# Performance work log

Hardware: AMD Instinct MI355X
Metric: run time of the kernel (lower is better)

## Reference

```python
import jax, jax.numpy as jnp
import numpy as np

N_NODES = 10000
N_EDGES = 160000
MUL = 128          # channel multiplicity
N_SPECIES = 10
SH_OFF = [0, 1, 4, 9, 16]   # spherical-harmonic offsets for l=0..3 (2l+1 each)
RADIAL_IN = 8
SIN_DIM = 32
MAX_DENSITY = 100.0


def setup_inputs() -> dict:
    key = jax.random.key(0)
    ks = jax.random.split(key, 16)
    inp = {
        'node_attrs': jax.random.normal(ks[0], (N_NODES, N_SPECIES), jnp.float32),
        'node_feats': jax.random.normal(ks[1], (N_NODES, MUL), jnp.float32),
        'edge_attrs': jax.random.normal(ks[2], (N_EDGES, 16), jnp.float32),
        'edge_feats': jax.random.normal(ks[3], (N_EDGES, RADIAL_IN), jnp.float32),
        'edge_index': jax.random.randint(ks[4], (2, N_EDGES), 0, N_NODES, jnp.int64),
        'W_up': jax.random.normal(ks[5], (MUL, MUL), jnp.float32),
        'Wr1': jax.random.normal(ks[6], (RADIAL_IN, 64), jnp.float32),
        'Wr2': jax.random.normal(ks[7], (64, 64), jnp.float32),
        'Wr3': jax.random.normal(ks[8], (64, 64), jnp.float32),
        'Wr4': jax.random.normal(ks[9], (64, 4 * MUL), jnp.float32),
        'Wd': jax.random.normal(ks[10], (RADIAL_IN, 1), jnp.float32),
        'Wsin': jax.random.normal(ks[11], (SIN_DIM, MUL), jnp.float32),
        'Wlin': jax.random.normal(ks[12], (4, MUL, MUL), jnp.float32),
        'Wskip': jax.random.normal(ks[13], (4, MUL, N_SPECIES, MUL), jnp.float32),
    }
    return inp


def _sinusoidal_embedding(x):
    # continuous sinusoidal embedding: dim=32, max_density=100
    half = SIN_DIM // 2
    freqs = jnp.exp(-jnp.log(MAX_DENSITY) * jnp.arange(half, dtype=x.dtype) / half)
    ang = x[:, None] * freqs[None, :]          # [N, 16]
    return jnp.concatenate([jnp.sin(ang), jnp.cos(ang)], axis=-1)  # [N, 32]


def reference(node_attrs, node_feats, edge_attrs, edge_feats, edge_index,
              W_up, Wr1, Wr2, Wr3, Wr4, Wd, Wsin, Wlin, Wskip):
    N = node_feats.shape[0]
    sender, receiver = edge_index[0], edge_index[1]

    # linear_up (e3nn o3.Linear on 128x0e, fan-in normalized)
    x = node_feats @ (W_up / np.float32(np.sqrt(MUL)))          # [N, 128]

    # radial MLP: FullyConnectedNet([8,64,64,64,512], silu), fan-in normalized
    h = edge_feats
    for W in (Wr1, Wr2, Wr3):
        h = jax.nn.silu(h @ (W / np.float32(np.sqrt(W.shape[0]))))
    tp_w = (h @ (Wr4 / np.float32(np.sqrt(64)))).reshape(-1, 4, MUL)  # [E, 4, 128]

    # equivariant TP: scalar node feats (x) gathered by sender, uvu path per SH l
    xs = x[sender]                                              # [E, 128]
    weighted = xs[:, None, :] * tp_w                            # [E, 4, 128]
    blocks = []
    for l in range(4):
        sh_l = edge_attrs[:, SH_OFF[l]:SH_OFF[l + 1]]           # [E, 2l+1]
        blk = weighted[:, l, :, None] * sh_l[:, None, :]        # [E, 128, 2l+1]
        blocks.append(blk.reshape(blk.shape[0], -1))
    mji = jnp.concatenate(blocks, axis=-1)                      # [E, 2048]

    # per-edge density gate
    density = jnp.tanh((edge_feats @ Wd) ** 2)                  # [E, 1]

    # scatter-sum messages and density to receivers
    message = jax.ops.segment_sum(mji, receiver, num_segments=N)        # [N, 2048]
    rho = jax.ops.segment_sum(density, receiver, num_segments=N)       # [N, 1]
    message = message / (rho + 1.0)

    # density embedding injected into the l=0 block
    demb = _sinusoidal_embedding(rho[:, 0]) @ Wsin              # [N, 128]
    message = message.at[:, :MUL].add(demb)

    # per-l linear (irreps_mid -> irreps_out), skip_tp with node_attrs, reshape
    out_blocks = []
    for l in range(4):
        d = 2 * l + 1
        blk = message[:, MUL * SH_OFF[l]:MUL * SH_OFF[l + 1]].reshape(N, MUL, d)
        blk = jnp.einsum('nuk,uv->nvk', blk, Wlin[l]) / np.float32(np.sqrt(MUL))
        blk = jnp.einsum('nvk,na,vaw->nwk', blk, node_attrs, Wskip[l]) \
              / np.float32(np.sqrt(MUL * N_SPECIES))
        out_blocks.append(blk)
    return jnp.concatenate(out_blocks, axis=-1)                 # [N, 128, 16]
```

## Files before the change

### kernel.cpp

```cpp
#include <hip/hip_runtime.h>
#include <hip/hip_bf16.h>

#define N_NODES 10000
#define N_EDGES 160000

typedef _Float16 h8 __attribute__((ext_vector_type(8)));
typedef _Float16 h4 __attribute__((ext_vector_type(4)));
typedef _Float16 h2 __attribute__((ext_vector_type(2)));
typedef float f32x4 __attribute__((ext_vector_type(4)));

__device__ __forceinline__ float silu_f(float v){ return v / (1.f + expf(-v)); }

__global__ __launch_bounds__(256) void k_node_up(const float* __restrict__ nf,
                                                 const _Float16* __restrict__ WupT,
                                                 float* __restrict__ x){
  const int n0 = blockIdx.x * 64;
  const int tid = threadIdx.x;
  alignas(16) __shared__ _Float16 s_nf[64*128];
  alignas(16) __shared__ _Float16 s_wt[128*128];

  {
    const int rl = tid >> 2, part = tid & 3;
    const int gr = n0 + rl;
    #pragma unroll
    for (int j = 0; j < 4; ++j){
      const int cu = part*4 + j;
      h8 hv = (h8){};
      if (gr < N_NODES){
        const float4 v0 = *(const float4*)(nf + (size_t)gr*128 + cu*8);
        const float4 v1 = *(const float4*)(nf + (size_t)gr*128 + cu*8 + 4);
        hv[0]=(_Float16)v0.x; hv[1]=(_Float16)v0.y; hv[2]=(_Float16)v0.z; hv[3]=(_Float16)v0.w;
        hv[4]=(_Float16)v1.x; hv[5]=(_Float16)v1.y; hv[6]=(_Float16)v1.z; hv[7]=(_Float16)v1.w;
      }
      const int cs = (cu & 8) | ((cu & 7) ^ (rl & 7));
      *(h8*)&s_nf[rl*128 + cs*8] = hv;
    }
  }
  {
    const int rl = tid >> 1, part = tid & 1;
    #pragma unroll
    for (int j = 0; j < 8; ++j){
      const int cu = part*8 + j;
      const h8 v = *(const h8*)&WupT[(size_t)rl*128 + cu*8];
      const int cs = (cu & 8) | ((cu & 7) ^ (rl & 7));
      *(h8*)&s_wt[rl*128 + cs*8] = v;
    }
  }
  __syncthreads();

  const int wid = tid >> 6, lane = tid & 63;
  const int li = lane & 15, kg = lane >> 4;

  f32x4 acc[8];
  #pragma unroll
  for (int i = 0; i < 8; ++i) acc[i] = (f32x4){0,0,0,0};

  const int row = wid*16 + li;
  #pragma unroll
  for (int s = 0; s < 4; ++s){
    const int ca = s*4 + kg;
    const int csA = (ca & 8) | ((ca & 7) ^ (row & 7));
    const h8 af = *(const h8*)&s_nf[row*128 + csA*8];
    #pragma unroll
    for (int nt = 0; nt < 8; ++nt){
      const int u = nt*16 + li;
      const int csB = (ca & 8) | ((ca & 7) ^ (u & 7));
      const h8 bf = *(const h8*)&s_wt[u*128 + csB*8];
      acc[nt] = __builtin_amdgcn_mfma_f32_16x16x32_f16(af, bf, acc[nt], 0, 0, 0);
    }
  }
  #pragma unroll
  for (int nt = 0; nt < 8; ++nt){
    #pragma unroll
    for (int r = 0; r < 4; ++r){
      const int gr = n0 + wid*16 + kg*4 + r;
      if (gr < N_NODES) x[(size_t)gr*128 + nt*16 + li] = acc[nt][r];
    }
  }
}

__global__ __launch_bounds__(256) void k_wc(const float* __restrict__ Wlin,
                                            const float* __restrict__ Wskip,
                                            _Float16* __restrict__ WC16T){
  const int lu = blockIdx.x;
  const int l  = lu >> 7, u = lu & 127;
  __shared__ float wl[128];
  if (threadIdx.x < 128) wl[threadIdx.x] = Wlin[lu*128 + threadIdx.x];
  __syncthreads();
  const float* Wsk = Wskip + (size_t)l * 163840;
  for (int i = threadIdx.x; i < 1280; i += 256){
    float acc = 0.f;
    #pragma unroll 16
    for (int v = 0; v < 128; ++v) acc += wl[v] * Wsk[v*1280 + i];
    const int a = i >> 7, w = i & 127;
    WC16T[((size_t)l*128 + w)*1280 + a*128 + u] =
        (_Float16)(acc * 0.0024705294220065465f);
  }
}

__global__ __launch_bounds__(256) void k_prep(const float* __restrict__ Wr2,
                                              const float* __restrict__ Wr3,
                                              const float* __restrict__ Wr4,
                                              const float* __restrict__ Wup,
                                              _Float16* __restrict__ Wr2T,
                                              _Float16* __restrict__ Wr3T,
                                              _Float16* __restrict__ Wr4T,
                                              _Float16* __restrict__ WupT){
  const int idx = blockIdx.x*256 + threadIdx.x;
  if (idx < 4096){
    const int n = idx >> 6, k = idx & 63;
    Wr2T[idx] = (_Float16)(Wr2[k*64 + n] * 0.125f);
  } else if (idx < 8192){
    const int j = idx - 4096;
    const int n = j >> 6, k = j & 63;
    Wr3T[j] = (_Float16)(Wr3[k*64 + n] * 0.125f);
  } else if (idx < 40960){
    const int j = idx - 8192;
    const int n = j >> 6, k = j & 63;
    Wr4T[j] = (_Float16)(Wr4[k*512 + n] * 0.125f);
  } else if (idx < 57344){
    const int j = idx - 40960;
    const int u = j >> 7, k = j & 127;
    WupT[j] = (_Float16)(Wup[k*128 + u] * 0.08838834764831843f);
  }
}

__global__ __launch_bounds__(256) void k_count(const int* __restrict__ eidx,
                                               int* __restrict__ cnt){
  const int e = blockIdx.x * 256 + threadIdx.x;
  if (e < N_EDGES) atomicAdd(&cnt[eidx[N_EDGES + e]], 1);
}

__global__ __launch_bounds__(256) void k_scan(const int* __restrict__ cnt,
                                              int* __restrict__ off,
                                              int* __restrict__ cur){
  __shared__ int sums[256];
  const int t = threadIdx.x;
  const int base = t * 40;
  int s = 0;
  for (int i = 0; i < 40; ++i){
    const int idx = base + i;
    if (idx < N_NODES) s += cnt[idx];
  }
  sums[t] = s;
  __syncthreads();
  for (int st = 1; st < 256; st <<= 1){
    const int v = (t >= st) ? sums[t - st] : 0;
    __syncthreads();
    sums[t] += v;
    __syncthreads();
  }
  int pre = (t > 0) ? sums[t - 1] : 0;
  for (int i = 0; i < 40; ++i){
    const int idx = base + i;
    if (idx < N_NODES){
      off[idx] = pre; cur[idx] = pre;
      pre += cnt[idx];
    }
  }
  if (t == 255) off[N_NODES] = sums[255];
}

__global__ __launch_bounds__(256) void k_bucket(const int* __restrict__ eidx,
                                                int* __restrict__ cur,
                                                int* __restrict__ elist,
                                                int* __restrict__ esnd){
  const int e = blockIdx.x * 256 + threadIdx.x;
  if (e < N_EDGES){
    const int pos = atomicAdd(&cur[eidx[N_EDGES + e]], 1);
    elist[pos] = e;
    esnd[pos]  = eidx[e];
  }
}

__global__ __launch_bounds__(256) void k_fused(const float* __restrict__ ef,
                                               const float* __restrict__ ea,
                                               const float* __restrict__ x,
                                               const float* __restrict__ Wr1,
                                               const float* __restrict__ Wd,
                                               const _Float16* __restrict__ Wr2T,
                                               const _Float16* __restrict__ Wr3T,
                                               const _Float16* __restrict__ Wr4T,
                                               const float* __restrict__ Wsin,
                                               const int* __restrict__ off,
                                               const int* __restrict__ elist,
                                               const int* __restrict__ esnd,
                                               float* __restrict__ msg){
  const int n0 = blockIdx.x * 4;
  const int tid = threadIdx.x;
  const int lane = tid & 63, wid = tid >> 6;
  const int li = lane & 15, kg = lane >> 4;
  const int u2 = tid & 63, q = tid >> 6;

  __shared__ int   s_eid[16];
  __shared__ float s_ef[16][8];
  __shared__ float s_w1[8][64];
  alignas(16) __shared__ _Float16 s_xs[16][136];
  alignas(16) __shared__ _Float16 s_actA[16][64];
  alignas(16) __shared__ _Float16 s_actB[16][64];
  alignas(16) __shared__ _Float16 s_w2[16][520];
  alignas(16) __shared__ float s_sh[16][16];
  __shared__ float s_dd[16];
  __shared__ float s_rho[4];
  __shared__ int   s_offs[5];
  __shared__ float s_emb[4][32];

  if (tid < 5) s_offs[tid] = off[n0 + tid];
  if (tid < 4) s_rho[tid] = 0.f;
  for (int j = tid; j < 512; j += 256) s_w1[j >> 6][j & 63] = Wr1[j];
  __syncthreads();

  const int beg = s_offs[0], end = s_offs[4];
  const int ngrp = (end - beg + 15) >> 4;

  float a0[8] = {0,0,0,0,0,0,0,0};
  float a1[8] = {0,0,0,0,0,0,0,0};
  float a2[8] = {0,0,0,0,0,0,0,0};
  float a3[8] = {0,0,0,0,0,0,0,0};

  for (int grp = 0; grp < ngrp; ++grp){
    const int pbase = beg + grp*16;

    if (tid < 16) s_eid[tid] = (pbase + tid < end) ? elist[pbase + tid] : -1;
    __syncthreads();

    if (tid < 128){
      const int e = tid >> 3, i = tid & 7;
      const int eid = s_eid[e];
      s_ef[e][i] = (eid >= 0) ? ef[(size_t)eid*8 + i] : 0.f;
    }
    {
      const int slot = tid >> 4, jj = tid & 15;
      const int eid = s_eid[slot];
      s_sh[slot][jj] = (eid >= 0) ? ea[(size_t)eid*16 + jj] : 0.f;
    }
    {
      const int e = tid >> 4, qq = tid & 15;
      const int p = pbase + e;
      const int snd = (p < end) ? esnd[p] : 0;
      const float4* xp = (const float4*)(x + (size_t)snd*128 + qq*8);
      const float4 v0 = xp[0], v1 = xp[1];
      h4 ha, hb;
      ha[0]=(_Float16)v0.x; ha[1]=(_Float16)v0.y; ha[2]=(_Float16)v0.z; ha[3]=(_Float16)v0.w;
      hb[0]=(_Float16)v1.x; hb[1]=(_Float16)v1.y; hb[2]=(_Float16)v1.z; hb[3]=(_Float16)v1.w;
      *(h4*)&s_xs[e][qq*8]     = ha;
      *(h4*)&s_xs[e][qq*8 + 4] = hb;
    }
    __syncthreads();

    if (tid < 16){
      float s = 0.f;
      #pragma unroll
      for (int i = 0; i < 8; ++i) s += s_ef[tid][i] * Wd[i];
      s_dd[tid] = tanhf(s*s);
    }

    {
      const int e = tid >> 4, ng = tid & 15;
      float hv[4] = {0,0,0,0};
      #pragma unroll
      for (int k = 0; k < 8; ++k){
        const float ev = s_ef[e][k] * 0.3535533905932738f;
        #pragma unroll
        for (int j = 0; j < 4; ++j) hv[j] += ev * s_w1[k][ng*4 + j];
      }
      h4 o;
      #pragma unroll
      for (int j = 0; j < 4; ++j) o[j] = (_Float16)silu_f(hv[j]);
      const int nb = ng*4;
      *(h4*)&s_actA[e][((nb >> 3) ^ (e & 7))*8 + (nb & 7)] = o;
    }
    __syncthreads();

    {
      h8 af[2];
      #pragma unroll
      for (int s = 0; s < 2; ++s)
        af[s] = *(const h8*)&Wr2T[(size_t)(wid*16 + li)*64 + s*32 + kg*8];
      f32x4 acc = (f32x4){0,0,0,0};
      #pragma unroll
      for (int s = 0; s < 2; ++s){
        const h8 bf = *(const h8*)&s_actA[li][((s*4 + kg) ^ (li & 7))*8];
        acc = __builtin_amdgcn_mfma_f32_16x16x32_f16(af[s], bf, acc, 0, 0, 0);
      }
      #pragma unroll
      for (int r = 0; r < 4; ++r){
        const int n = wid*16 + kg*4 + r;
        s_actB[li][((n >> 3) ^ (li & 7))*8 + (n & 7)] = (_Float16)silu_f(acc[r]);
      }
    }
    __syncthreads();

    {
      h8 af[2];
      #pragma unroll
      for (int s = 0; s < 2; ++s)
        af[s] = *(const h8*)&Wr3T[(size_t)(wid*16 + li)*64 + s*32 + kg*8];
      f32x4 acc = (f32x4){0,0,0,0};
      #pragma unroll
      for (int s = 0; s < 2; ++s){
        const h8 bf = *(const h8*)&s_actB[li][((s*4 + kg) ^ (li & 7))*8];
        acc = __builtin_amdgcn_mfma_f32_16x16x32_f16(af[s], bf, acc, 0, 0, 0);
      }
      #pragma unroll
      for (int r = 0; r < 4; ++r){
        const int n = wid*16 + kg*4 + r;
        s_actA[li][((n >> 3) ^ (li & 7))*8 + (n & 7)] = (_Float16)silu_f(acc[r]);
      }
    }
    __syncthreads();

    {
      h8 bf[2];
      #pragma unroll
      for (int s = 0; s < 2; ++s)
        bf[s] = *(const h8*)&s_actA[li][((s*4 + kg) ^ (li & 7))*8];
      #pragma unroll
      for (int mt = 0; mt < 8; ++mt){
        const int nbase = wid*128 + mt*16;
        h8 af[2];
        #pragma unroll
        for (int s = 0; s < 2; ++s)
          af[s] = *(const h8*)&Wr4T[(size_t)(nbase + li)*64 + s*32 + kg*8];
        f32x4 acc = (f32x4){0,0,0,0};
        #pragma unroll
        for (int s = 0; s < 2; ++s)
          acc = __builtin_amdgcn_mfma_f32_16x16x32_f16(af[s], bf[s], acc, 0, 0, 0);
        const int c0 = nbase + kg*4;
        const int u0 = c0 & 127;
        const h4 xv = *(const h4*)&s_xs[li][u0];
        h4 ov;
        #pragma unroll
        for (int r = 0; r < 4; ++r) ov[r] = (_Float16)acc[r] * xv[r];
        *(h4*)&s_w2[li][c0] = ov;
      }
    }
    __syncthreads();

    int lo0 = s_offs[0] - pbase; lo0 = lo0 < 0 ? 0 : lo0;
    int hi0 = s_offs[1] - pbase; hi0 = hi0 > 16 ? 16 : (hi0 < 0 ? 0 : hi0);
    int lo1 = s_offs[1] - pbase; lo1 = lo1 < 0 ? 0 : lo1;
    int hi1 = s_offs[2] - pbase; hi1 = hi1 > 16 ? 16 : (hi1 < 0 ? 0 : hi1);
    int lo2 = s_offs[2] - pbase; lo2 = lo2 < 0 ? 0 : lo2;
    int hi2 = s_offs[3] - pbase; hi2 = hi2 > 16 ? 16 : (hi2 < 0 ? 0 : hi2);
    int lo3 = s_offs[3] - pbase; lo3 = lo3 < 0 ? 0 : lo3;
    int hi3 = s_offs[4] - pbase; hi3 = hi3 > 16 ? 16 : (hi3 < 0 ? 0 : hi3);

#define ACCQ0(A, LO, HI)                                             \
    for (int s = (LO); s < (HI); ++s){                               \
      const h2 w0 = *(const h2*)&s_w2[s][2*u2];                      \
      const h2 w1 = *(const h2*)&s_w2[s][128 + 2*u2];                \
      const float4 sv = *(const float4*)&s_sh[s][0];                 \
      A[0] += (float)w0[0]*sv.x; A[1] += (float)w0[1]*sv.x;          \
      A[2] += (float)w1[0]*sv.y; A[3] += (float)w1[1]*sv.y;          \
      A[4] += (float)w1[0]*sv.z; A[5] += (float)w1[1]*sv.z;          \
      A[6] += (float)w1[0]*sv.w; A[7] += (float)w1[1]*sv.w;          \
    }
#define ACCQ1(A, LO, HI)                                             \
    for (int s = (LO); s < (HI); ++s){                               \
      const h2 wv = *(const h2*)&s_w2[s][256 + 2*u2];                \
      const float4 sv = *(const float4*)&s_sh[s][4];                 \
      A[0] += (float)wv[0]*sv.x; A[1] += (float)wv[1]*sv.x;          \
      A[2] += (float)wv[0]*sv.y; A[3] += (float)wv[1]*sv.y;          \
      A[4] += (float)wv[0]*sv.z; A[5] += (float)wv[1]*sv.z;          \
      A[6] += (float)wv[0]*sv.w; A[7] += (float)wv[1]*sv.w;          \
    }
#define ACCQ2(A, LO, HI)                                             \
    for (int s = (LO); s < (HI); ++s){                               \
      const h2 wv = *(const h2*)&s_w2[s][256 + 2*u2];                \
      const h2 wx = *(const h2*)&s_w2[s][384 + 2*u2];                \
      const float4 sv = *(const float4*)&s_sh[s][8];                 \
      A[0] += (float)wv[0]*sv.x; A[1] += (float)wv[1]*sv.x;          \
      A[2] += (float)wx[0]*sv.y; A[3] += (float)wx[1]*sv.y;          \
      A[4] += (float)wx[0]*sv.z; A[5] += (float)wx[1]*sv.z;          \
      A[6] += (float)wx[0]*sv.w; A[7] += (float)wx[1]*sv.w;          \
    }
#define ACCQ3(A, LO, HI)                                             \
    for (int s = (LO); s < (HI); ++s){                               \
      const h2 wx = *(const h2*)&s_w2[s][384 + 2*u2];                \
      const float4 sv = *(const float4*)&s_sh[s][12];                \
      A[0] += (float)wx[0]*sv.x; A[1] += (float)wx[1]*sv.x;          \
      A[2] += (float)wx[0]*sv.y; A[3] += (float)wx[1]*sv.y;          \
      A[4] += (float)wx[0]*sv.z; A[5] += (float)wx[1]*sv.z;          \
      A[6] += (float)wx[0]*sv.w; A[7] += (float)wx[1]*sv.w;          \
    }

    if (q == 0){
      ACCQ0(a0, lo0, hi0) ACCQ0(a1, lo1, hi1) ACCQ0(a2, lo2, hi2) ACCQ0(a3, lo3, hi3)
    } else if (q == 1){
      ACCQ1(a0, lo0, hi0) ACCQ1(a1, lo1, hi1) ACCQ1(a2, lo2, hi2) ACCQ1(a3, lo3, hi3)
    } else if (q == 2){
      ACCQ2(a0, lo0, hi0) ACCQ2(a1, lo1, hi1) ACCQ2(a2, lo2, hi2) ACCQ2(a3, lo3, hi3)
    } else {
      ACCQ3(a0, lo0, hi0) ACCQ3(a1, lo1, hi1) ACCQ3(a2, lo2, hi2) ACCQ3(a3, lo3, hi3)
    }

    if (tid < 4){
      int lo = s_offs[tid]     - pbase; lo = lo < 0 ? 0 : lo;
      int hi = s_offs[tid + 1] - pbase; hi = hi > 16 ? 16 : (hi < 0 ? 0 : hi);
      float r = 0.f;
      for (int s = lo; s < hi; ++s) r += s_dd[s];
      s_rho[tid] += r;
    }
    __syncthreads();
  }

  if (tid < 64){
    const int ni = tid >> 4, f = tid & 15;
    const float fr  = expf(-0.28782313662425572f * (float)f);
    const float ang = s_rho[ni] * fr;
    s_emb[ni][f]      = sinf(ang);
    s_emb[ni][f + 16] = cosf(ang);
  }
  __syncthreads();

  float db00=0.f, db01=0.f, db10=0.f, db11=0.f;
  float db20=0.f, db21=0.f, db30=0.f, db31=0.f;
  if (q == 0){
    #pragma unroll 8
    for (int j = 0; j < 32; ++j){
      const float w0 = Wsin[j*128 + 2*u2];
      const float w1 = Wsin[j*128 + 2*u2 + 1];
      const float e0 = s_emb[0][j], e1 = s_emb[1][j];
      const float e2 = s_emb[2][j], e3 = s_emb[3][j];
      db00 += e0*w0; db01 += e0*w1;
      db10 += e1*w0; db11 += e1*w1;
      db20 += e2*w0; db21 += e2*w1;
      db30 += e3*w0; db31 += e3*w1;
    }
  }
  const float t0 = 1.f/(s_rho[0]+1.f), t1 = 1.f/(s_rho[1]+1.f);
  const float t2 = 1.f/(s_rho[2]+1.f), t3 = 1.f/(s_rho[3]+1.f);

  #pragma unroll
  for (int j = 0; j < 4; ++j){
    const int sk = q*4 + j;
    const size_t base = (size_t)sk*128 + 2*u2;
    float2 v0 = { a0[j*2+0]*t0, a0[j*2+1]*t0 };
    float2 v1 = { a1[j*2+0]*t1, a1[j*2+1]*t1 };
    float2 v2 = { a2[j*2+0]*t2, a2[j*2+1]*t2 };
    float2 v3 = { a3[j*2+0]*t3, a3[j*2+1]*t3 };
    if (q == 0 && j == 0){
      v0.x += db00; v0.y += db01;
      v1.x += db10; v1.y += db11;
      v2.x += db20; v2.y += db21;
      v3.x += db30; v3.y += db31;
    }
    *(float2*)&msg[(size_t)(n0+0)*2048 + base] = v0;
    *(float2*)&msg[(size_t)(n0+1)*2048 + base] = v1;
    *(float2*)&msg[(size_t)(n0+2)*2048 + base] = v2;
    *(float2*)&msg[(size_t)(n0+3)*2048 + base] = v3;
  }
}

template<int L, int D>
__device__ __forceinline__ void final_body(const int bb,
                                           const float* __restrict__ msg,
                                           const float* __restrict__ attrs,
                                           const _Float16* __restrict__ WC16T,
                                           float* __restrict__ outD,
                                           _Float16* __restrict__ sA,
                                           _Float16* __restrict__ sB,
                                           _Float16* __restrict__ sAttr){
  constexpr int OFF  = (L==0 ? 0 : L==1 ? 1 : L==2 ? 4 : 9);
  constexpr int ROWS = N_NODES * D;
  const int r0  = bb * 128;
  const int tid = threadIdx.x;

  {
    const int rl = tid >> 1, half = tid & 1;
    const int gr = r0 + rl;
    h8 vals[8];
    if (gr < ROWS){
      const int n = gr / D, k = gr - n*D;
      const float4* src = (const float4*)(msg + (size_t)n*2048 + (size_t)(OFF+k)*128 + half*64);
      #pragma unroll
      for (int j = 0; j < 8; ++j){
        const float4 v0 = src[j*2], v1 = src[j*2+1];
        h8 hv;
        hv[0]=(_Float16)v0.x; hv[1]=(_Float16)v0.y; hv[2]=(_Float16)v0.z; hv[3]=(_Float16)v0.w;
        hv[4]=(_Float16)v1.x; hv[5]=(_Float16)v1.y; hv[6]=(_Float16)v1.z; hv[7]=(_Float16)v1.w;
        vals[j] = hv;
      }
    } else {
      #pragma unroll
      for (int j = 0; j < 8; ++j) vals[j] = (h8){};
    }
    #pragma unroll
    for (int j = 0; j < 8; ++j){
      const int cu = half*8 + j;
      const int cs = (cu & 8) | ((cu & 7) ^ (rl & 7));
      *(h8*)&sA[rl*128 + cs*8] = vals[j];
    }
  }
  for (int i = tid; i < 1280; i += 256){
    const int rl = i / 10, aa = i - rl*10;
    const int gr = r0 + rl;
    sAttr[i] = (gr < ROWS) ? (_Float16)attrs[(gr / D)*10 + aa] : (_Float16)0.f;
  }
  {
    const int w = tid >> 1, part = tid & 1;
    const _Float16* src = WC16T + ((size_t)L*128 + w)*1280 + part*32;
    #pragma unroll
    for (int j = 0; j < 4; ++j){
      const h8 v = *(const h8*)(src + j*8);
      const int cc = part*4 + j;
      *(h8*)&sB[w*64 + (cc ^ (w & 7))*8] = v;
    }
  }
  __syncthreads();

  const int wid = tid >> 6, lane = tid & 63;
  const int wm = wid >> 1, wn = wid & 1;
  const int li = lane & 15, kg = lane >> 4;

  f32x4 acc[4][4];
  #pragma unroll
  for (int m = 0; m < 4; ++m)
    #pragma unroll
    for (int nn = 0; nn < 4; ++nn) acc[m][nn] = (f32x4){0,0,0,0};

  for (int step = 0; step < 20; ++step){
    _Float16* sbc = (step & 1) ? (sB + 8192) : sB;
    _Float16* sbn = (step & 1) ? sB : (sB + 8192);
    const bool more = (step + 1 < 20);
    h8 pre[4];
    if (more){
      const int a2 = (step+1) >> 1, u02 = ((step+1) & 1) << 6;
      const _Float16* src = WC16T + ((size_t)L*128 + (tid>>1))*1280 + a2*128 + u02 + (tid&1)*32;
      #pragma unroll
      for (int j = 0; j < 4; ++j) pre[j] = *(const h8*)(src + j*8);
    }

    const int a  = step >> 1;
    const int uh = (step & 1) << 3;

    h8 afr[4][2], bfr[4][2];
    #pragma unroll
    for (int m = 0; m < 4; ++m){
      const int row = wm*64 + m*16 + li;
      const _Float16 av = sAttr[row*10 + a];
      h8 avx;
      #pragma unroll
      for (int j = 0; j < 8; ++j) avx[j] = av;
      #pragma unroll
      for (int s = 0; s < 2; ++s){
        const int ca = uh + s*4 + kg;
        const int cs = (ca & 8) | ((ca & 7) ^ (row & 7));
        const h8 mA = *(const h8*)&sA[row*128 + cs*8];
        afr[m][s] = mA * avx;
      }
    }
    #pragma unroll
    for (int nn = 0; nn < 4; ++nn){
      const int w = wn*64 + nn*16 + li;
      #pragma unroll
      for (int s = 0; s < 2; ++s){
        const int cb = s*4 + kg;
        bfr[nn][s] = *(const h8*)&sbc[w*64 + ((cb ^ (w & 7)))*8];
      }
    }
    #pragma unroll
    for (int s = 0; s < 2; ++s)
      #pragma unroll
      for (int m = 0; m < 4; ++m)
        #pragma unroll
        for (int nn = 0; nn < 4; ++nn)
          acc[m][nn] = __builtin_amdgcn_mfma_f32_16x16x32_f16(afr[m][s], bfr[nn][s], acc[m][nn], 0, 0, 0);

    if (more){
      const int w = tid >> 1, part = tid & 1;
      #pragma unroll
      for (int j = 0; j < 4; ++j){
        const int cc = part*4 + j;
        *(h8*)&sbn[w*64 + (cc ^ (w & 7))*8] = pre[j];
      }
    }
    __syncthreads();
  }

  #pragma unroll
  for (int m = 0; m < 4; ++m){
    const int rbase = r0 + wm*64 + m*16 + kg*4;
    #pragma unroll
    for (int rr = 0; rr < 4; ++rr){
      const int gr = rbase + rr;
      if (gr < ROWS){
        float* op = outD + (size_t)gr*128;
        #pragma unroll
        for (int nn = 0; nn < 4; ++nn)
          op[wn*64 + nn*16 + li] = acc[m][nn][rr];
      }
    }
  }
}

__global__ __launch_bounds__(256) void k_final_all(const float* __restrict__ msg,
                                                   const float* __restrict__ attrs,
                                                   const _Float16* __restrict__ WC16T,
                                                   float* __restrict__ outD){
  alignas(16) __shared__ _Float16 sA[128*128];
  alignas(16) __shared__ _Float16 sB[2*64*128];
  __shared__ _Float16 sAttr[128*10];
  const int b = blockIdx.x;
  if (b < 79)       final_body<0,1>(b,       msg, attrs, WC16T, outD,            sA, sB, sAttr);
  else if (b < 314) final_body<1,3>(b - 79,  msg, attrs, WC16T, outD + 1280000,  sA, sB, sAttr);
  else if (b < 705) final_body<2,5>(b - 314, msg, attrs, WC16T, outD + 5120000,  sA, sB, sAttr);
  else              final_body<3,7>(b - 705, msg, attrs, WC16T, outD + 11520000, sA, sB, sAttr);
}

__global__ __launch_bounds__(256) void k_merge(const float* __restrict__ outD,
                                               float* __restrict__ out){
  const int n0 = blockIdx.x * 4;
  const int tid = threadIdx.x;
  __shared__ float lds[4*16*132];

  {
    const float4* src = (const float4*)(outD + (size_t)n0*128);
    for (int j = tid; j < 128; j += 256){
      const int row = j >> 5, c4 = j & 31;
      *(float4*)&lds[(row*16 + 0)*132 + c4*4] = src[j];
    }
  }
  {
    const float4* src = (const float4*)(outD + 1280000 + (size_t)n0*3*128);
    for (int j = tid; j < 384; j += 256){
      const int row = j >> 5, c4 = j & 31;
      const int nloc = row/3, k = row - nloc*3;
      *(float4*)&lds[(nloc*16 + 1 + k)*132 + c4*4] = src[j];
    }
  }
  {
    const float4* src = (const float4*)(outD + 5120000 + (size_t)n0*5*128);
    for (int j = tid; j < 640; j += 256){
      const int row = j >> 5, c4 = j & 31;
      const int nloc = row/5, k = row - nloc*5;
      *(float4*)&lds[(nloc*16 + 4 + k)*132 + c4*4] = src[j];
    }
  }
  {
    const float4* src = (const float4*)(outD + 11520000 + (size_t)n0*7*128);
    for (int j = tid; j < 896; j += 256){
      const int row = j >> 5, c4 = j & 31;
      const int nloc = row/7, k = row - nloc*7;
      *(float4*)&lds[(nloc*16 + 9 + k)*132 + c4*4] = src[j];
    }
  }
  __syncthreads();

  for (int j = tid; j < 2048; j += 256){
    const int nloc = j >> 9, qv = j & 511;
    const int w = qv >> 2, s0 = (qv & 3) << 2;
    float4 v;
    v.x = lds[(nloc*16 + s0 + 0)*132 + w];
    v.y = lds[(nloc*16 + s0 + 1)*132 + w];
    v.z = lds[(nloc*16 + s0 + 2)*132 + w];
    v.w = lds[(nloc*16 + s0 + 3)*132 + w];
    *(float4*)&out[(size_t)(n0 + nloc)*2048 + qv*4] = v;
  }
}

extern "C" void kernel_launch(void* const* d_in, const int* in_sizes, int n_in,
                              void* d_out, int out_size, void* d_ws, size_t ws_size,
                              hipStream_t stream){
  const float* node_attrs = (const float*)d_in[0];
  const float* node_feats = (const float*)d_in[1];
  const float* edge_attrs = (const float*)d_in[2];
  const float* edge_feats = (const float*)d_in[3];
  const int*   edge_index = (const int*)d_in[4];
  const float* W_up  = (const float*)d_in[5];
  const float* Wr1   = (const float*)d_in[6];
  const float* Wr2   = (const float*)d_in[7];
  const float* Wr3   = (const float*)d_in[8];
  const float* Wr4   = (const float*)d_in[9];
  const float* Wd    = (const float*)d_in[10];
  const float* Wsin  = (const float*)d_in[11];
  const float* Wlin  = (const float*)d_in[12];
  const float* Wskip = (const float*)d_in[13];
  float* out = (float*)d_out;

  float* outD    = (float*)d_ws;
  float* msg     = outD + 20480000;
  float* x       = msg + 20480000;
  _Float16* WC16T= (_Float16*)(x + 1280000);
  int* cnt   = (int*)(WC16T + 655360);
  int* off   = cnt + 10000;
  int* cur   = off + 10016;
  int* elist = cur + 10000;
  int* esnd  = elist + 160000;
  _Float16* Wr2T = (_Float16*)(esnd + 160000);
  _Float16* Wr3T = Wr2T + 4096;
  _Float16* Wr4T = Wr3T + 4096;
  _Float16* WupT = Wr4T + 32768;

  hipMemsetAsync(cnt, 0, (size_t)10000 * sizeof(int), stream);

  k_prep<<<224, 256, 0, stream>>>(Wr2, Wr3, Wr4, W_up, Wr2T, Wr3T, Wr4T, WupT);
  k_node_up<<<157, 256, 0, stream>>>(node_feats, WupT, x);
  k_wc<<<512, 256, 0, stream>>>(Wlin, Wskip, WC16T);

  k_count <<<(N_EDGES + 255)/256, 256, 0, stream>>>(edge_index, cnt);
  k_scan  <<<1, 256, 0, stream>>>(cnt, off, cur);
  k_bucket<<<(N_EDGES + 255)/256, 256, 0, stream>>>(edge_index, cur, elist, esnd);

  k_fused<<<N_NODES/4, 256, 0, stream>>>(edge_feats, edge_attrs, x,
                                         Wr1, Wd, Wr2T, Wr3T, Wr4T, Wsin,
                                         off, elist, esnd, msg);

  k_final_all<<<1252, 256, 0, stream>>>(msg, node_attrs, WC16T, outD);

  k_merge<<<2500, 256, 0, stream>>>(outD, out);
}
```

Baseline: 368.7 us.

## Process 32 edges per group in fused edge kernel and merge weight-prep kernels

The fused edge kernel now handles 32 edges per iteration instead of 16. Each radial-MLP weight fragment loaded from global memory is reused across two MFMA edge tiles, and the number of block-wide barriers per edge is halved. The s_actB buffer is aliased onto s_w2 to save LDS, at the cost of a larger LDS footprint and more padded slots when a node group has few edges. The two weight-preparation kernels are merged into one launch to remove one launch's overhead.

Result: slower. 446.6 us (+21.1%).

```diff
diff --git a/kernel.cpp b/kernel.cpp
--- a/kernel.cpp
+++ b/kernel.cpp
@@ -10,6 +10,54 @@
 typedef float f32x4 __attribute__((ext_vector_type(4)));
 
 __device__ __forceinline__ float silu_f(float v){ return v / (1.f + expf(-v)); }
+
+__global__ __launch_bounds__(256) void k_pre(const float* __restrict__ Wr2,
+                                             const float* __restrict__ Wr3,
+                                             const float* __restrict__ Wr4,
+                                             const float* __restrict__ Wup,
+                                             const float* __restrict__ Wlin,
+                                             const float* __restrict__ Wskip,
+                                             _Float16* __restrict__ Wr2T,
+                                             _Float16* __restrict__ Wr3T,
+                                             _Float16* __restrict__ Wr4T,
+                                             _Float16* __restrict__ WupT,
+                                             _Float16* __restrict__ WC16T){
+  const int b = blockIdx.x;
+  __shared__ float wl[128];
+  if (b < 224){
+    const int idx = b*256 + threadIdx.x;
+    if (idx < 4096){
+      const int n = idx >> 6, k = idx & 63;
+      Wr2T[idx] = (_Float16)(Wr2[k*64 + n] * 0.125f);
+    } else if (idx < 8192){
+      const int j = idx - 4096;
+      const int n = j >> 6, k = j & 63;
+      Wr3T[j] = (_Float16)(Wr3[k*64 + n] * 0.125f);
+    } else if (idx < 40960){
+      const int j = idx - 8192;
+      const int n = j >> 6, k = j & 63;
+      Wr4T[j] = (_Float16)(Wr4[k*512 + n] * 0.125f);
+    } else if (idx < 57344){
+      const int j = idx - 40960;
+      const int u = j >> 7, k = j & 127;
+      WupT[j] = (_Float16)(Wup[k*128 + u] * 0.08838834764831843f);
+    }
+  } else {
+    const int lu = b - 224;
+    const int l  = lu >> 7, u = lu & 127;
+    if (threadIdx.x < 128) wl[threadIdx.x] = Wlin[lu*128 + threadIdx.x];
+    __syncthreads();
+    const float* Wsk = Wskip + (size_t)l * 163840;
+    for (int i = threadIdx.x; i < 1280; i += 256){
+      float acc = 0.f;
+      #pragma unroll 16
+      for (int v = 0; v < 128; ++v) acc += wl[v] * Wsk[v*1280 + i];
+      const int a = i >> 7, w = i & 127;
+      WC16T[((size_t)l*128 + w)*1280 + a*128 + u] =
+          (_Float16)(acc * 0.0024705294220065465f);
+    }
+  }
+}
 
 __global__ __launch_bounds__(256) void k_node_up(const float* __restrict__ nf,
                                                  const _Float16* __restrict__ WupT,
@@ -76,52 +124,6 @@
       const int gr = n0 + wid*16 + kg*4 + r;
       if (gr < N_NODES) x[(size_t)gr*128 + nt*16 + li] = acc[nt][r];
     }
-  }
-}
-
-__global__ __launch_bounds__(256) void k_wc(const float* __restrict__ Wlin,
-                                            const float* __restrict__ Wskip,
-                                            _Float16* __restrict__ WC16T){
-  const int lu = blockIdx.x;
-  const int l  = lu >> 7, u = lu & 127;
-  __shared__ float wl[128];
-  if (threadIdx.x < 128) wl[threadIdx.x] = Wlin[lu*128 + threadIdx.x];
-  __syncthreads();
-  const float* Wsk = Wskip + (size_t)l * 163840;
-  for (int i = threadIdx.x; i < 1280; i += 256){
-    float acc = 0.f;
-    #pragma unroll 16
-    for (int v = 0; v < 128; ++v) acc += wl[v] * Wsk[v*1280 + i];
-    const int a = i >> 7, w = i & 127;
-    WC16T[((size_t)l*128 + w)*1280 + a*128 + u] =
-        (_Float16)(acc * 0.0024705294220065465f);
-  }
-}
-
-__global__ __launch_bounds__(256) void k_prep(const float* __restrict__ Wr2,
-                                              const float* __restrict__ Wr3,
-                                              const float* __restrict__ Wr4,
-                                              const float* __restrict__ Wup,
-                                              _Float16* __restrict__ Wr2T,
-                                              _Float16* __restrict__ Wr3T,
-                                              _Float16* __restrict__ Wr4T,
-                                              _Float16* __restrict__ WupT){
-  const int idx = blockIdx.x*256 + threadIdx.x;
-  if (idx < 4096){
-    const int n = idx >> 6, k = idx & 63;
-    Wr2T[idx] = (_Float16)(Wr2[k*64 + n] * 0.125f);
-  } else if (idx < 8192){
-    const int j = idx - 4096;
-    const int n = j >> 6, k = j & 63;
-    Wr3T[j] = (_Float16)(Wr3[k*64 + n] * 0.125f);
-  } else if (idx < 40960){
-    const int j = idx - 8192;
-    const int n = j >> 6, k = j & 63;
-    Wr4T[j] = (_Float16)(Wr4[k*512 + n] * 0.125f);
-  } else if (idx < 57344){
-    const int j = idx - 40960;
-    const int u = j >> 7, k = j & 127;
-    WupT[j] = (_Float16)(Wup[k*128 + u] * 0.08838834764831843f);
   }
 }
 
@@ -192,18 +194,19 @@
   const int li = lane & 15, kg = lane >> 4;
   const int u2 = tid & 63, q = tid >> 6;
 
-  __shared__ int   s_eid[16];
-  __shared__ float s_ef[16][8];
+  __shared__ int   s_eid[32];
+  __shared__ float s_ef[32][8];
   __shared__ float s_w1[8][64];
-  alignas(16) __shared__ _Float16 s_xs[16][136];
-  alignas(16) __shared__ _Float16 s_actA[16][64];
-  alignas(16) __shared__ _Float16 s_actB[16][64];
-  alignas(16) __shared__ _Float16 s_w2[16][520];
-  alignas(16) __shared__ float s_sh[16][16];
-  __shared__ float s_dd[16];
+  alignas(16) __shared__ _Float16 s_xs[32][132];
+  alignas(16) __shared__ _Float16 s_actA[32][64];
+  alignas(16) __shared__ _Float16 s_w2[32][520];
+  alignas(16) __shared__ float s_sh[32][16];
+  __shared__ float s_dd[32];
   __shared__ float s_rho[4];
   __shared__ int   s_offs[5];
   __shared__ float s_emb[4][32];
+
+  _Float16* s_actB = &s_w2[0][0];
 
   if (tid < 5) s_offs[tid] = off[n0 + tid];
   if (tid < 4) s_rho[tid] = 0.f;
@@ -211,7 +214,7 @@
   __syncthreads();
 
   const int beg = s_offs[0], end = s_offs[4];
-  const int ngrp = (end - beg + 15) >> 4;
+  const int ngrp = (end - beg + 31) >> 5;
 
   float a0[8] = {0,0,0,0,0,0,0,0};
   float a1[8] = {0,0,0,0,0,0,0,0};
@@ -219,36 +222,38 @@
   float a3[8] = {0,0,0,0,0,0,0,0};
 
   for (int grp = 0; grp < ngrp; ++grp){
-    const int pbase = beg + grp*16;
-
-    if (tid < 16) s_eid[tid] = (pbase + tid < end) ? elist[pbase + tid] : -1;
-    __syncthreads();
-
-    if (tid < 128){
+    const int pbase = beg + grp*32;
+
+    if (tid < 32) s_eid[tid] = (pbase + tid < end) ? elist[pbase + tid] : -1;
+    __syncthreads();
+
+    {
       const int e = tid >> 3, i = tid & 7;
       const int eid = s_eid[e];
       s_ef[e][i] = (eid >= 0) ? ef[(size_t)eid*8 + i] : 0.f;
     }
-    {
-      const int slot = tid >> 4, jj = tid & 15;
+    #pragma unroll
+    for (int c2 = 0; c2 < 2; ++c2){
+      const int idx = c2*256 + tid;
+      const int slot = idx >> 4, jj = idx & 15;
       const int eid = s_eid[slot];
       s_sh[slot][jj] = (eid >= 0) ? ea[(size_t)eid*16 + jj] : 0.f;
     }
     {
-      const int e = tid >> 4, qq = tid & 15;
+      const int e = tid >> 3, qq = tid & 7;
       const int p = pbase + e;
       const int snd = (p < end) ? esnd[p] : 0;
-      const float4* xp = (const float4*)(x + (size_t)snd*128 + qq*8);
-      const float4 v0 = xp[0], v1 = xp[1];
-      h4 ha, hb;
-      ha[0]=(_Float16)v0.x; ha[1]=(_Float16)v0.y; ha[2]=(_Float16)v0.z; ha[3]=(_Float16)v0.w;
-      hb[0]=(_Float16)v1.x; hb[1]=(_Float16)v1.y; hb[2]=(_Float16)v1.z; hb[3]=(_Float16)v1.w;
-      *(h4*)&s_xs[e][qq*8]     = ha;
-      *(h4*)&s_xs[e][qq*8 + 4] = hb;
-    }
-    __syncthreads();
-
-    if (tid < 16){
+      const float4* xp = (const float4*)(x + (size_t)snd*128 + qq*16);
+      #pragma unroll
+      for (int j = 0; j < 4; ++j){
+        const float4 v = xp[j];
+        h4 hv; hv[0]=(_Float16)v.x; hv[1]=(_Float16)v.y; hv[2]=(_Float16)v.z; hv[3]=(_Float16)v.w;
+        *(h4*)&s_xs[e][qq*16 + j*4] = hv;
+      }
+    }
+    __syncthreads();
+
+    if (tid < 32){
       float s = 0.f;
       #pragma unroll
       for (int i = 0; i < 8; ++i) s += s_ef[tid][i] * Wd[i];
@@ -256,19 +261,18 @@
     }
 
     {
-      const int e = tid >> 4, ng = tid & 15;
-      float hv[4] = {0,0,0,0};
+      const int e = tid >> 3, ng = tid & 7;
+      float hv[8] = {0,0,0,0,0,0,0,0};
       #pragma unroll
       for (int k = 0; k < 8; ++k){
         const float ev = s_ef[e][k] * 0.3535533905932738f;
         #pragma unroll
-        for (int j = 0; j < 4; ++j) hv[j] += ev * s_w1[k][ng*4 + j];
-      }
-      h4 o;
-      #pragma unroll
-      for (int j = 0; j < 4; ++j) o[j] = (_Float16)silu_f(hv[j]);
-      const int nb = ng*4;
-      *(h4*)&s_actA[e][((nb >> 3) ^ (e & 7))*8 + (nb & 7)] = o;
+        for (int j = 0; j < 8; ++j) hv[j] += ev * s_w1[k][ng*8 + j];
+      }
+      h8 o;
+      #pragma unroll
+      for (int j = 0; j < 8; ++j) o[j] = (_Float16)silu_f(hv[j]);
+      *(h8*)&s_actA[e][(ng ^ (e & 7))*8] = o;
     }
     __syncthreads();
 
@@ -277,16 +281,20 @@
       #pragma unroll
       for (int s = 0; s < 2; ++s)
         af[s] = *(const h8*)&Wr2T[(size_t)(wid*16 + li)*64 + s*32 + kg*8];
-      f32x4 acc = (f32x4){0,0,0,0};
-      #pragma unroll
-      for (int s = 0; s < 2; ++s){
-        const h8 bf = *(const h8*)&s_actA[li][((s*4 + kg) ^ (li & 7))*8];
-        acc = __builtin_amdgcn_mfma_f32_16x16x32_f16(af[s], bf, acc, 0, 0, 0);
-      }
-      #pragma unroll
-      for (int r = 0; r < 4; ++r){
-        const int n = wid*16 + kg*4 + r;
-        s_actB[li][((n >> 3) ^ (li & 7))*8 + (n & 7)] = (_Float16)silu_f(acc[r]);
+      #pragma unroll
+      for (int nt = 0; nt < 2; ++nt){
+        const int e = nt*16 + li;
+        f32x4 acc = (f32x4){0,0,0,0};
+        #pragma unroll
+        for (int s = 0; s < 2; ++s){
+          const h8 bf = *(const h8*)&s_actA[e][((s*4 + kg) ^ (e & 7))*8];
+          acc = __builtin_amdgcn_mfma_f32_16x16x32_f16(af[s], bf, acc, 0, 0, 0);
+        }
+        #pragma unroll
+        for (int r = 0; r < 4; ++r){
+          const int n = wid*16 + kg*4 + r;
+          s_actB[e*64 + ((n >> 3) ^ (e & 7))*8 + (n & 7)] = (_Float16)silu_f(acc[r]);
+        }
       }
     }
     __syncthreads();
@@ -296,55 +304,74 @@
       #pragma unroll
       for (int s = 0; s < 2; ++s)
         af[s] = *(const h8*)&Wr3T[(size_t)(wid*16 + li)*64 + s*32 + kg*8];
-      f32x4 acc = (f32x4){0,0,0,0};
-      #pragma unroll
-      for (int s = 0; s < 2; ++s){
-        const h8 bf = *(const h8*)&s_actB[li][((s*4 + kg) ^ (li & 7))*8];
-        acc = __builtin_amdgcn_mfma_f32_16x16x32_f16(af[s], bf, acc, 0, 0, 0);
-      }
-      #pragma unroll
-      for (int r = 0; r < 4; ++r){
-        const int n = wid*16 + kg*4 + r;
-        s_actA[li][((n >> 3) ^ (li & 7))*8 + (n & 7)] = (_Float16)silu_f(acc[r]);
+      #pragma unroll
+      for (int nt = 0; nt < 2; ++nt){
+        const int e = nt*16 + li;
+        f32x4 acc = (f32x4){0,0,0,0};
+        #pragma unroll
+        for (int s = 0; s < 2; ++s){
+          const h8 bf = *(const h8*)&s_actB[e*64 + ((s*4 + kg) ^ (e & 7))*8];
+          acc = __builtin_amdgcn_mfma_f32_16x16x32_f16(af[s], bf, acc, 0, 0, 0);
+        }
+        #pragma unroll
+        for (int r = 0; r < 4; ++r){
+          const int n = wid*16 + kg*4 + r;
+          s_actA[e][((n >> 3) ^ (e & 7))*8 + (n & 7)] = (_Float16)silu_f(acc[r]);
+        }
       }
     }
     __syncthreads();
 
     {
-      h8 bf[2];
-      #pragma unroll
-      for (int s = 0; s < 2; ++s)
-        bf[s] = *(const h8*)&s_actA[li][((s*4 + kg) ^ (li & 7))*8];
-      #pragma unroll
-      for (int mt = 0; mt < 8; ++mt){
-        const int nbase = wid*128 + mt*16;
-        h8 af[2];
+      h8 bf[2][2];
+      #pragma unroll
+      for (int nt = 0; nt < 2; ++nt){
+        const int e = nt*16 + li;
         #pragma unroll
         for (int s = 0; s < 2; ++s)
-          af[s] = *(const h8*)&Wr4T[(size_t)(nbase + li)*64 + s*32 + kg*8];
-        f32x4 acc = (f32x4){0,0,0,0};
-        #pragma unroll
-        for (int s = 0; s < 2; ++s)
-          acc = __builtin_amdgcn_mfma_f32_16x16x32_f16(af[s], bf[s], acc, 0, 0, 0);
-        const int c0 = nbase + kg*4;
-        const int u0 = c0 & 127;
-        const h4 xv = *(const h4*)&s_xs[li][u0];
-        h4 ov;
-        #pragma unroll
-        for (int r = 0; r < 4; ++r) ov[r] = (_Float16)acc[r] * xv[r];
-        *(h4*)&s_w2[li][c0] = ov;
+          bf[nt][s] = *(const h8*)&s_actA[e][((s*4 + kg) ^ (e & 7))*8];
+      }
+      #pragma unroll
+      for (int p = 0; p < 2; ++p){
+        #pragma unroll
+        for (int mt = 0; mt < 4; ++mt){
+          const int nbase = wid*128 + p*64 + mt*16;
+          h8 af[2];
+          #pragma unroll
+          for (int s = 0; s < 2; ++s)
+            af[s] = *(const h8*)&Wr4T[(size_t)(nbase + li)*64 + s*32 + kg*8];
+          f32x4 acc[2];
+          #pragma unroll
+          for (int nt = 0; nt < 2; ++nt){
+            acc[nt] = (f32x4){0,0,0,0};
+            #pragma unroll
+            for (int s = 0; s < 2; ++s)
+              acc[nt] = __builtin_amdgcn_mfma_f32_16x16x32_f16(af[s], bf[nt][s], acc[nt], 0, 0, 0);
+          }
+          const int c0 = nbase + kg*4;
+          const int u0 = c0 & 127;
+          #pragma unroll
+          for (int nt = 0; nt < 2; ++nt){
+            const int e = nt*16 + li;
+            const h4 xv = *(const h4*)&s_xs[e][u0];
+            h4 ov;
+            #pragma unroll
+            for (int r = 0; r < 4; ++r) ov[r] = (_Float16)acc[nt][r] * xv[r];
+            *(h4*)&s_w2[e][c0] = ov;
+          }
+        }
       }
     }
     __syncthreads();
 
     int lo0 = s_offs[0] - pbase; lo0 = lo0 < 0 ? 0 : lo0;
-    int hi0 = s_offs[1] - pbase; hi0 = hi0 > 16 ? 16 : (hi0 < 0 ? 0 : hi0);
+    int hi0 = s_offs[1] - pbase; hi0 = hi0 > 32 ? 32 : (hi0 < 0 ? 0 : hi0);
     int lo1 = s_offs[1] - pbase; lo1 = lo1 < 0 ? 0 : lo1;
-    int hi1 = s_offs[2] - pbase; hi1 = hi1 > 16 ? 16 : (hi1 < 0 ? 0 : hi1);
+    int hi1 = s_offs[2] - pbase; hi1 = hi1 > 32 ? 32 : (hi1 < 0 ? 0 : hi1);
     int lo2 = s_offs[2] - pbase; lo2 = lo2 < 0 ? 0 : lo2;
-    int hi2 = s_offs[3] - pbase; hi2 = hi2 > 16 ? 16 : (hi2 < 0 ? 0 : hi2);
+    int hi2 = s_offs[3] - pbase; hi2 = hi2 > 32 ? 32 : (hi2 < 0 ? 0 : hi2);
     int lo3 = s_offs[3] - pbase; lo3 = lo3 < 0 ? 0 : lo3;
-    int hi3 = s_offs[4] - pbase; hi3 = hi3 > 16 ? 16 : (hi3 < 0 ? 0 : hi3);
+    int hi3 = s_offs[4] - pbase; hi3 = hi3 > 32 ? 32 : (hi3 < 0 ? 0 : hi3);
 
 #define ACCQ0(A, LO, HI)                                             \
     for (int s = (LO); s < (HI); ++s){                               \
@@ -397,7 +424,7 @@
 
     if (tid < 4){
       int lo = s_offs[tid]     - pbase; lo = lo < 0 ? 0 : lo;
-      int hi = s_offs[tid + 1] - pbase; hi = hi > 16 ? 16 : (hi < 0 ? 0 : hi);
+      int hi = s_offs[tid + 1] - pbase; hi = hi > 32 ? 32 : (hi < 0 ? 0 : hi);
       float r = 0.f;
       for (int s = lo; s < hi; ++s) r += s_dd[s];
       s_rho[tid] += r;
@@ -695,9 +722,9 @@
 
   hipMemsetAsync(cnt, 0, (size_t)10000 * sizeof(int), stream);
 
-  k_prep<<<224, 256, 0, stream>>>(Wr2, Wr3, Wr4, W_up, Wr2T, Wr3T, Wr4T, WupT);
+  k_pre<<<736, 256, 0, stream>>>(Wr2, Wr3, Wr4, W_up, Wlin, Wskip,
+                                 Wr2T, Wr3T, Wr4T, WupT, WC16T);
   k_node_up<<<157, 256, 0, stream>>>(node_feats, WupT, x);
-  k_wc<<<512, 256, 0, stream>>>(Wlin, Wskip, WC16T);
 
   k_count <<<(N_EDGES + 255)/256, 256, 0, stream>>>(edge_index, cnt);
   k_scan  <<<1, 256, 0, stream>>>(cnt, off, cur);
```
